# Kernel optimization log

Hardware: AMD Instinct MI355X
Metric: run time of the kernel (lower is better)

Reference implementation:

```python
import jax, jax.numpy as jnp
import numpy as np

B = 8            # sequences
APPEND = 4096    # tokens appended per sequence
PAGE = 16        # page_size
PAGES_PER_SEQ = APPEND // PAGE  # 256
NPAGES = B * PAGES_PER_SEQ      # 2048
H, D = 8, 128


def setup_inputs() -> dict:
    key = jax.random.key(0)
    k1, k2 = jax.random.split(key)
    T = B * APPEND
    k = jax.random.normal(k1, (T, H, D), dtype=jnp.float32)
    v = jax.random.normal(k2, (T, H, D), dtype=jnp.float32)
    kv_cache = jnp.zeros((NPAGES, 2, PAGE, H, D), dtype=jnp.float32)
    kv_append_indptr = jnp.arange(B + 1, dtype=jnp.int32) * APPEND
    kv_page_indices = jnp.arange(NPAGES, dtype=jnp.int32)
    kv_page_indptr = jnp.arange(B + 1, dtype=jnp.int32) * PAGES_PER_SEQ
    kv_page_lastlen = jnp.full((B,), PAGE, dtype=jnp.int32)  # last page full
    return {
        "k": k, "v": v, "kv_cache": kv_cache,
        "kv_append_indptr": kv_append_indptr,
        "kv_page_indices": kv_page_indices,
        "kv_page_indptr": kv_page_indptr,
        "kv_page_lastlen": kv_page_lastlen,
    }


def reference(k, v, kv_cache, kv_append_indptr, kv_page_indices,
              kv_page_indptr, kv_page_lastlen):
    # Paged KV append (flashinfer append_paged_kv_cache semantics):
    # tokens k[indptr[b]:indptr[b+1]] fill the LAST append_len slots of
    # sequence b's page list, whose total occupied length is
    # (npages_b - 1) * page_size + lastlen_b.
    T = k.shape[0]
    P = kv_cache.shape[2]
    tok = jnp.arange(T, dtype=jnp.int32)
    b = (jnp.searchsorted(kv_append_indptr, tok, side="right") - 1).astype(jnp.int32)
    i = tok - kv_append_indptr[b]                       # local token idx
    npages = kv_page_indptr[b + 1] - kv_page_indptr[b]
    total_len = (npages - 1) * P + kv_page_lastlen[b]
    append_len = kv_append_indptr[b + 1] - kv_append_indptr[b]
    pos = total_len - append_len + i                    # position in seq's pages
    page = kv_page_indices[kv_page_indptr[b] + pos // P]
    slot = pos % P
    cache = kv_cache.at[page, 0, slot].set(k)
    cache = cache.at[page, 1, slot].set(v)
    return cache
```

## Files before the change

### kernel.cpp

```cpp
#include <hip/hip_runtime.h>


constexpr int B_      = 8;
constexpr int APPEND_ = 4096;
constexpr int PAGE_   = 16;
constexpr int H_      = 8;
constexpr int D_      = 128;
constexpr int HD      = H_ * D_;
constexpr int HD4     = HD / 4;
constexpr int T_      = B_ * APPEND_;
constexpr int N4      = T_ * HD4;
constexpr int PAGE_STRIDE4 = 2 * PAGE_ * HD4;
constexpr int V_OFF4       = PAGE_ * HD4;
constexpr int SLOT_STRIDE4 = HD4;

__global__ __launch_bounds__(256) void kv_append_kernel(
    const float4* __restrict__ k,
    const float4* __restrict__ v,
    float4* __restrict__ out,
    const int* __restrict__ kv_append_indptr,
    const int* __restrict__ kv_page_indices,
    const int* __restrict__ kv_page_indptr,
    const int* __restrict__ kv_page_lastlen)
{
    const int stride = gridDim.x * blockDim.x;
    for (int idx = blockIdx.x * blockDim.x + threadIdx.x; idx < N4; idx += stride) {
        const int t = idx >> 8;
        const int r = idx & (HD4 - 1);

        int b = 0;
        #pragma unroll
        for (int s = 0; s < B_ - 1; ++s) {
            b += (kv_append_indptr[s + 1] <= t) ? 1 : 0;
        }
        const int i = t - kv_append_indptr[b];

        const int p0        = kv_page_indptr[b];
        const int npages    = kv_page_indptr[b + 1] - p0;
        const int total_len = (npages - 1) * PAGE_ + kv_page_lastlen[b];
        const int app_len   = kv_append_indptr[b + 1] - kv_append_indptr[b];
        const int pos       = total_len - app_len + i;

        const int page = kv_page_indices[p0 + (pos >> 4)];
        const int slot = pos & (PAGE_ - 1);

        const float4 kq = k[idx];
        const float4 vq = v[idx];

        const int dst = page * PAGE_STRIDE4 + slot * SLOT_STRIDE4 + r;
        out[dst]          = kq;
        out[dst + V_OFF4] = vq;
    }
}

extern "C" void kernel_launch(void* const* d_in, const int* in_sizes, int n_in,
                              void* d_out, int out_size, void* d_ws, size_t ws_size,
                              hipStream_t stream) {
    const float4* k = (const float4*)d_in[0];
    const float4* v = (const float4*)d_in[1];
    const int* kv_append_indptr = (const int*)d_in[3];
    const int* kv_page_indices  = (const int*)d_in[4];
    const int* kv_page_indptr   = (const int*)d_in[5];
    const int* kv_page_lastlen  = (const int*)d_in[6];
    float4* out = (float4*)d_out;

    dim3 grid(2048), block(256);
    hipLaunchKernelGGL(kv_append_kernel, grid, block, 0, stream,
                       k, v, out,
                       kv_append_indptr, kv_page_indices,
                       kv_page_indptr, kv_page_lastlen);
}
```

Measured before the change: 541.3 us.

## Map one block per cache page and copy contiguous slot ranges

Replaces the per-float4 grid-stride loop, which recomputed the sequence search and page lookup for every element, with one block per page. Each block computes the page's metadata once, then copies the page's contiguous K and V slot range with unrolled float4 loads and stores. It launches one block per page based on the page_indices size and leaves pages outside the append range untouched. This relies on the k buffer for the appended tokens being contiguous per page.

```diff
diff --git a/kernel.cpp b/kernel.cpp
--- a/kernel.cpp
+++ b/kernel.cpp
@@ -1,20 +1,15 @@
 #include <hip/hip_runtime.h>
 
 
-constexpr int B_      = 8;
-constexpr int APPEND_ = 4096;
-constexpr int PAGE_   = 16;
-constexpr int H_      = 8;
-constexpr int D_      = 128;
-constexpr int HD      = H_ * D_;
-constexpr int HD4     = HD / 4;
-constexpr int T_      = B_ * APPEND_;
-constexpr int N4      = T_ * HD4;
-constexpr int PAGE_STRIDE4 = 2 * PAGE_ * HD4;
-constexpr int V_OFF4       = PAGE_ * HD4;
-constexpr int SLOT_STRIDE4 = HD4;
+constexpr int B_    = 8;
+constexpr int PAGE_ = 16;
+constexpr int H_    = 8;
+constexpr int D_    = 128;
+constexpr int HD4   = H_ * D_ / 4;
+constexpr int PAGE_ELEMS4   = PAGE_ * HD4;
+constexpr int PAGE_STRIDE4  = 2 * PAGE_ELEMS4;
 
-__global__ __launch_bounds__(256) void kv_append_kernel(
+__global__ __launch_bounds__(256) void kv_append_page_kernel(
     const float4* __restrict__ k,
     const float4* __restrict__ v,
     float4* __restrict__ out,
@@ -23,33 +18,45 @@
     const int* __restrict__ kv_page_indptr,
     const int* __restrict__ kv_page_lastlen)
 {
-    const int stride = gridDim.x * blockDim.x;
-    for (int idx = blockIdx.x * blockDim.x + threadIdx.x; idx < N4; idx += stride) {
-        const int t = idx >> 8;
-        const int r = idx & (HD4 - 1);
+    const int gpid = blockIdx.x;
+    const int tid  = threadIdx.x;
 
-        int b = 0;
-        #pragma unroll
-        for (int s = 0; s < B_ - 1; ++s) {
-            b += (kv_append_indptr[s + 1] <= t) ? 1 : 0;
+    int b = 0;
+    #pragma unroll
+    for (int s = 0; s < B_ - 1; ++s)
+        b += (kv_page_indptr[s + 1] <= gpid) ? 1 : 0;
+
+    const int p_local   = gpid - kv_page_indptr[b];
+    const int page      = kv_page_indices[gpid];
+    const int npages    = kv_page_indptr[b + 1] - kv_page_indptr[b];
+    const int total_len = (npages - 1) * PAGE_ + kv_page_lastlen[b];
+    const int app_start = kv_append_indptr[b];
+    const int app_len   = kv_append_indptr[b + 1] - app_start;
+    const int append_pos0 = total_len - app_len;
+
+    const int base_pos = p_local * PAGE_;
+    const int slot_lo = max(0, append_pos0 - base_pos);
+    const int slot_hi = min(PAGE_, total_len - base_pos);
+    const int off_lo  = slot_lo * HD4;
+    const int off_hi  = slot_hi * HD4;
+
+    const long long src_base = (long long)(app_start + base_pos - append_pos0) * HD4;
+    const int dst_base = page * PAGE_STRIDE4;
+
+    if (off_lo == 0 && off_hi == PAGE_ELEMS4) {
+        #pragma unroll 4
+        for (int off = tid; off < PAGE_ELEMS4; off += 256) {
+            out[dst_base + off]               = k[src_base + off];
+            out[dst_base + PAGE_ELEMS4 + off] = v[src_base + off];
         }
-        const int i = t - kv_append_indptr[b];
-
-        const int p0        = kv_page_indptr[b];
-        const int npages    = kv_page_indptr[b + 1] - p0;
-        const int total_len = (npages - 1) * PAGE_ + kv_page_lastlen[b];
-        const int app_len   = kv_append_indptr[b + 1] - kv_append_indptr[b];
-        const int pos       = total_len - app_len + i;
-
-        const int page = kv_page_indices[p0 + (pos >> 4)];
-        const int slot = pos & (PAGE_ - 1);
-
-        const float4 kq = k[idx];
-        const float4 vq = v[idx];
-
-        const int dst = page * PAGE_STRIDE4 + slot * SLOT_STRIDE4 + r;
-        out[dst]          = kq;
-        out[dst + V_OFF4] = vq;
+    } else {
+        #pragma unroll 4
+        for (int off = tid; off < PAGE_ELEMS4; off += 256) {
+            if (off >= off_lo && off < off_hi) {
+                out[dst_base + off]               = k[src_base + off];
+                out[dst_base + PAGE_ELEMS4 + off] = v[src_base + off];
+            }
+        }
     }
 }
 
@@ -64,8 +71,9 @@
     const int* kv_page_lastlen  = (const int*)d_in[6];
     float4* out = (float4*)d_out;
 
-    dim3 grid(2048), block(256);
-    hipLaunchKernelGGL(kv_append_kernel, grid, block, 0, stream,
+    const int npages_total = in_sizes[4];
+    dim3 grid(npages_total), block(256);
+    hipLaunchKernelGGL(kv_append_page_kernel, grid, block, 0, stream,
                        k, v, out,
                        kv_append_indptr, kv_page_indices,
                        kv_page_indptr, kv_page_lastlen);
```

Result: no change. 539.4 us (-0.4%).
